# Performance work log

Measured on AMD Instinct MI355X. Metric: run time of the kernel, lower is better.

## Reference

```python
import jax, jax.numpy as jnp
import numpy as np

HID = 2560
NH, P, N, G, K = 80, 64, 128, 1, 4
INTER = NH * P            # 5120
CONV_DIM = INTER + 2 * G * N  # 5376
PROJ = INTER + CONV_DIM + NH  # 10576
EPS = 1e-5
DT_MIN, DT_MAX = 0.0, 100.0
BATCH = 64


def setup_inputs() -> dict:
    key = jax.random.key(0)
    ks = jax.random.split(key, 11)
    return {
        "input_states": jax.random.normal(ks[0], (BATCH, 1, HID), jnp.float32),
        "conv_state": 0.1 * jax.random.normal(ks[1], (BATCH, CONV_DIM, K), jnp.float32),
        "ssm_state": 0.1 * jax.random.normal(ks[2], (BATCH, NH, P, N), jnp.float32),
        "in_proj_w": jax.random.normal(ks[3], (PROJ, HID), jnp.float32) * (HID ** -0.5),
        "conv_w": jax.random.normal(ks[4], (CONV_DIM, K), jnp.float32) * 0.2,
        "conv_b": jax.random.normal(ks[5], (CONV_DIM,), jnp.float32) * 0.02,
        "dt_bias": jax.random.normal(ks[6], (NH,), jnp.float32) * 0.1,
        "A_log": jnp.log(jnp.arange(1, NH + 1, dtype=jnp.float32)),
        "D": jnp.ones((NH,), jnp.float32),
        "norm_w": jnp.ones((INTER,), jnp.float32),
        "out_proj_w": jax.random.normal(ks[7], (HID, INTER), jnp.float32) * (INTER ** -0.5),
    }


def reference(input_states, conv_state, ssm_state, in_proj_w, conv_w, conv_b,
              dt_bias, A_log, D, norm_w, out_proj_w):
    B = input_states.shape[0]
    # in_proj: (B,1,HID) @ (HID,PROJ) -> (B,1,PROJ); d_mlp == 0 with these dims
    proj = jnp.einsum("bsh,ph->bsp", input_states, in_proj_w)
    gate = proj[..., :INTER]                       # (B,1,INTER)
    hBC = proj[..., INTER:INTER + CONV_DIM]        # (B,1,CONV_DIM)
    dt = proj[..., INTER + CONV_DIM:]              # (B,1,NH)

    # conv cache update: roll left, append current token
    new_conv_state = jnp.concatenate(
        [conv_state[:, :, 1:], hBC[:, 0, :, None]], axis=-1)  # (B,CONV_DIM,K)
    x = jnp.sum(new_conv_state * conv_w[None], axis=-1) + conv_b  # (B,CONV_DIM)
    x = jax.nn.silu(x)

    hs = x[:, :INTER].reshape(B, NH, P)            # (B,NH,P)
    Bm = x[:, INTER:INTER + G * N].reshape(B, G, N)
    Cm = x[:, INTER + G * N:].reshape(B, G, N)
    Bm = jnp.repeat(Bm, NH // G, axis=1)           # (B,NH,N)
    Cm = jnp.repeat(Cm, NH // G, axis=1)           # (B,NH,N)

    # discretization (dt is per-head, broadcast over head_dim as in source)
    dt_sp = jnp.clip(jax.nn.softplus(dt[:, 0, :] + dt_bias), DT_MIN, DT_MAX)  # (B,NH)
    A = -jnp.exp(A_log)                            # (NH,)
    dA = jnp.exp(dt_sp * A)                        # (B,NH)

    dBx = dt_sp[:, :, None, None] * Bm[:, :, None, :] * hs[..., None]  # (B,NH,P,N)
    new_ssm = ssm_state * dA[:, :, None, None] + dBx                   # (B,NH,P,N)

    y = jnp.einsum("bhpn,bhn->bhp", new_ssm, Cm)   # (B,NH,P)
    y = y + hs * D[None, :, None]
    y = y.reshape(B, 1, INTER)

    # gated RMSNorm (fp32 internals)
    yf = y.astype(jnp.float32) * jax.nn.silu(gate.astype(jnp.float32))
    var = jnp.mean(yf * yf, axis=-1, keepdims=True)
    yn = norm_w * (yf * jax.lax.rsqrt(var + EPS)).astype(y.dtype)

    out = jnp.einsum("bsi,hi->bsh", yn, out_proj_w)  # (B,1,HID)
    return out
```

## Files before the change

### kernel.cpp

```cpp
#include <hip/hip_runtime.h>
#include <stdint.h>

#define HID 2560
#define NH 80
#define PDIM 64
#define NDIM 128
#define INTER 5120
#define CONV_DIM 5376
#define PROJ_DIM 10576
#define NBATCH 64
#define EPS_ 1e-5f

typedef short short8 __attribute__((ext_vector_type(8)));
typedef float f32x4 __attribute__((ext_vector_type(4)));

__device__ __forceinline__ unsigned short f2bf(float f){
  unsigned u = __builtin_bit_cast(unsigned, f);
  u += 0x7FFFu + ((u >> 16) & 1u);
  return (unsigned short)(u >> 16);
}
__device__ __forceinline__ float silu_(float x){ return x / (1.f + __expf(-x)); }

__global__ __launch_bounds__(256) void k_dt(const float* __restrict__ X,
                                            const float* __restrict__ W,
                                            float* __restrict__ dt_part,
                                            unsigned short* __restrict__ Xb){
  const int h = blockIdx.x, ks = blockIdx.y;
  const int tid = threadIdx.x, wid = tid >> 6, lane = tid & 63;
  const float* wr = W + (size_t)(INTER + CONV_DIM + h) * HID + ks * 320;
  float w[5];
  #pragma unroll
  for (int i = 0; i < 5; ++i) w[i] = wr[lane + i * 64];
  #pragma unroll
  for (int bi = 0; bi < 16; ++bi){
    const int b = wid * 16 + bi;
    const float* xr = X + (size_t)b * HID + ks * 320;
    float x[5];
    float acc = 0.f;
    #pragma unroll
    for (int i = 0; i < 5; ++i){ x[i] = xr[lane + i * 64]; acc += x[i] * w[i]; }
    if (h == 0){
      #pragma unroll
      for (int i = 0; i < 5; ++i)
        Xb[(size_t)b * HID + ks * 320 + lane + i * 64] = f2bf(x[i]);
    }
    #pragma unroll
    for (int m = 32; m; m >>= 1) acc += __shfl_xor(acc, m);
    if (lane == 0) dt_part[(ks * NBATCH + b) * NH + h] = acc;
  }
}

__global__ __launch_bounds__(64, 1) void k1_proj(const unsigned short* __restrict__ Xb,
                                                 const float* __restrict__ W,
                                                 float* __restrict__ pp){
  const int lane = threadIdx.x;
  const int lr = lane & 15, lg = lane >> 4;
  const int n0 = blockIdx.x * 16;
  const int ks = blockIdx.y;
  const int kb = ks * 640;
  const short* ap = (const short*)Xb + (size_t)lr * HID + kb + lg * 8;
  const float* bp = W + (size_t)(n0 + lr) * HID + kb + lg * 8;
  f32x4 acc0 = {0,0,0,0}, acc1 = {0,0,0,0}, acc2 = {0,0,0,0}, acc3 = {0,0,0,0};
  short8 A0[4], A1[4], A2[4], A3[4];
  float4 B0[4], B1[4];
  #pragma unroll
  for (int p = 0; p < 4; ++p){
    const int k = p * 32;
    A0[p] = *(const short8*)(ap + k);
    A1[p] = *(const short8*)(ap + 16 * HID + k);
    A2[p] = *(const short8*)(ap + 32 * HID + k);
    A3[p] = *(const short8*)(ap + 48 * HID + k);
    B0[p] = *(const float4*)(bp + k);
    B1[p] = *(const float4*)(bp + k + 4);
  }
  #pragma unroll 4
  for (int s = 0; s < 16; ++s){
    const int p = s & 3;
    short8 bb;
    bb[0]=(short)f2bf(B0[p].x); bb[1]=(short)f2bf(B0[p].y);
    bb[2]=(short)f2bf(B0[p].z); bb[3]=(short)f2bf(B0[p].w);
    bb[4]=(short)f2bf(B1[p].x); bb[5]=(short)f2bf(B1[p].y);
    bb[6]=(short)f2bf(B1[p].z); bb[7]=(short)f2bf(B1[p].w);
    acc0 = __builtin_amdgcn_mfma_f32_16x16x32_bf16(A0[p], bb, acc0, 0, 0, 0);
    acc1 = __builtin_amdgcn_mfma_f32_16x16x32_bf16(A1[p], bb, acc1, 0, 0, 0);
    acc2 = __builtin_amdgcn_mfma_f32_16x16x32_bf16(A2[p], bb, acc2, 0, 0, 0);
    acc3 = __builtin_amdgcn_mfma_f32_16x16x32_bf16(A3[p], bb, acc3, 0, 0, 0);
    const int k = (s + 4) * 32;
    A0[p] = *(const short8*)(ap + k);
    A1[p] = *(const short8*)(ap + 16 * HID + k);
    A2[p] = *(const short8*)(ap + 32 * HID + k);
    A3[p] = *(const short8*)(ap + 48 * HID + k);
    B0[p] = *(const float4*)(bp + k);
    B1[p] = *(const float4*)(bp + k + 4);
  }
  #pragma unroll
  for (int s = 16; s < 20; ++s){
    const int p = s & 3;
    short8 bb;
    bb[0]=(short)f2bf(B0[p].x); bb[1]=(short)f2bf(B0[p].y);
    bb[2]=(short)f2bf(B0[p].z); bb[3]=(short)f2bf(B0[p].w);
    bb[4]=(short)f2bf(B1[p].x); bb[5]=(short)f2bf(B1[p].y);
    bb[6]=(short)f2bf(B1[p].z); bb[7]=(short)f2bf(B1[p].w);
    acc0 = __builtin_amdgcn_mfma_f32_16x16x32_bf16(A0[p], bb, acc0, 0, 0, 0);
    acc1 = __builtin_amdgcn_mfma_f32_16x16x32_bf16(A1[p], bb, acc1, 0, 0, 0);
    acc2 = __builtin_amdgcn_mfma_f32_16x16x32_bf16(A2[p], bb, acc2, 0, 0, 0);
    acc3 = __builtin_amdgcn_mfma_f32_16x16x32_bf16(A3[p], bb, acc3, 0, 0, 0);
  }
  float* plane = pp + (size_t)ks * NBATCH * PROJ_DIM;
  #pragma unroll
  for (int r = 0; r < 4; ++r){
    const int m = lg * 4 + r;
    plane[(size_t)(m     ) * PROJ_DIM + n0 + lr] = acc0[r];
    plane[(size_t)(m + 16) * PROJ_DIM + n0 + lr] = acc1[r];
    plane[(size_t)(m + 32) * PROJ_DIM + n0 + lr] = acc2[r];
    plane[(size_t)(m + 48) * PROJ_DIM + n0 + lr] = acc3[r];
  }
}

__global__ __launch_bounds__(256) void k2a(const float* __restrict__ cs,
                                           const float* __restrict__ cw,
                                           const float* __restrict__ cb,
                                           const float* __restrict__ pp,
                                           const float* __restrict__ dt_part,
                                           const float* __restrict__ dt_bias,
                                           const float* __restrict__ A_log,
                                           float* __restrict__ hs_bc,
                                           float* __restrict__ dt_sp,
                                           float* __restrict__ dAv,
                                           float* __restrict__ s_bc){
  const int b = blockIdx.y;
  const int c0 = blockIdx.x * 384;
  const int tid = threadIdx.x;
  const size_t plane = (size_t)NBATCH * PROJ_DIM;
  __shared__ float bc[384];
  for (int i = tid; i < 384; i += 256){
    const int c = c0 + i;
    float4 s4 = *(const float4*)(cs + ((size_t)b * CONV_DIM + c) * 4);
    float4 w4 = *(const float4*)(cw + (size_t)c * 4);
    const size_t pidx = (size_t)b * PROJ_DIM + INTER + c;
    float hbc = pp[pidx] + pp[plane + pidx] + pp[2*plane + pidx] + pp[3*plane + pidx];
    float x = s4.y * w4.x + s4.z * w4.y + s4.w * w4.z + hbc * w4.w + cb[c];
    float v = silu_(x);
    hs_bc[(size_t)b * CONV_DIM + c] = v;
    if (blockIdx.x == 13) bc[i] = v;
  }
  if (blockIdx.x == 0 && tid < NH){
    float acc = dt_bias[tid];
    #pragma unroll
    for (int ks = 0; ks < 8; ++ks) acc += dt_part[(ks * NBATCH + b) * NH + tid];
    float sp = acc > 15.f ? acc : log1pf(__expf(acc));
    sp = fminf(fmaxf(sp, 0.f), 100.f);
    dt_sp[b * NH + tid] = sp;
    dAv[b * NH + tid] = __expf(-sp * __expf(A_log[tid]));
  }
  if (blockIdx.x == 13){
    __syncthreads();
    if (tid < 64){
      float p = bc[128 + tid] * bc[256 + tid] + bc[192 + tid] * bc[320 + tid];
      #pragma unroll
      for (int m = 32; m; m >>= 1) p += __shfl_xor(p, m);
      if (tid == 0) s_bc[b] = p;
    }
  }
}

__global__ __launch_bounds__(256) void k2b(const float* __restrict__ ssm,
                                           const float* __restrict__ hs_bc,
                                           const float* __restrict__ pp,
                                           const float* __restrict__ dt_sp,
                                           const float* __restrict__ dAv,
                                           const float* __restrict__ s_bc,
                                           const float* __restrict__ Dp,
                                           const float* __restrict__ norm_w,
                                           unsigned short* __restrict__ yfb,
                                           float* __restrict__ ssq_part){
  const int h = blockIdx.x, b = blockIdx.y;
  const int tid = threadIdx.x;
  const int wid = tid >> 6, lane = tid & 63;
  const int lr = lane & 15, lg = lane >> 4;
  const float dA_s = dAv[b * NH + h];
  const float coef = dt_sp[b * NH + h] * s_bc[b] + Dp[h];
  const size_t plane = (size_t)NBATCH * PROJ_DIM;
  const float* Cb = hs_bc + (size_t)b * CONV_DIM + INTER + NDIM;
  float4 c0 = *(const float4*)(Cb + lr * 8);
  float4 c1 = *(const float4*)(Cb + lr * 8 + 4);
  const float* srow = ssm + ((size_t)b * NH + h) * PDIM * NDIM;
  float ssq = 0.f;
  __shared__ float ssql[4];
  #pragma unroll
  for (int r = 0; r < 4; ++r){
    const int p = wid * 16 + r * 4 + lg;
    const float* sp_ = srow + (size_t)p * NDIM + lr * 8;
    float4 v0 = *(const float4*)(sp_);
    float4 v1 = *(const float4*)(sp_ + 4);
    float dot = v0.x*c0.x + v0.y*c0.y + v0.z*c0.z + v0.w*c0.w
              + v1.x*c1.x + v1.y*c1.y + v1.z*c1.z + v1.w*c1.w;
    dot += __shfl_xor(dot, 1); dot += __shfl_xor(dot, 2);
    dot += __shfl_xor(dot, 4); dot += __shfl_xor(dot, 8);
    if (lr == 0){
      const int hp = h * PDIM + p;
      float hs = hs_bc[(size_t)b * CONV_DIM + hp];
      float y = dA_s * dot + hs * coef;
      const size_t gi = (size_t)b * PROJ_DIM + hp;
      float g = pp[gi] + pp[plane + gi] + pp[2*plane + gi] + pp[3*plane + gi];
      float yf = y * silu_(g) * norm_w[hp];
      yfb[(size_t)b * INTER + hp] = f2bf(yf);
      ssq += yf * yf;
    }
  }
  #pragma unroll
  for (int m = 32; m; m >>= 1) ssq += __shfl_xor(ssq, m);
  if (lane == 0) ssql[wid] = ssq;
  __syncthreads();
  if (tid == 0) ssq_part[b * NH + h] = ssql[0] + ssql[1] + ssql[2] + ssql[3];
}

__global__ __launch_bounds__(64, 1) void k3_out(const unsigned short* __restrict__ Yb,
                                                const float* __restrict__ W,
                                                float* __restrict__ part){
  const int lane = threadIdx.x;
  const int lr = lane & 15, lg = lane >> 4;
  const int n0 = blockIdx.x * 16;
  const int ks = blockIdx.y;
  const int kb = ks * 1280;
  const short* ap = (const short*)Yb + (size_t)lr * INTER + kb + lg * 8;
  const float* bp = W + (size_t)(n0 + lr) * INTER + kb + lg * 8;
  f32x4 acc0 = {0,0,0,0}, acc1 = {0,0,0,0}, acc2 = {0,0,0,0}, acc3 = {0,0,0,0};
  short8 A0[4], A1[4], A2[4], A3[4];
  float4 B0[4], B1[4];
  #pragma unroll
  for (int p = 0; p < 4; ++p){
    const int k = p * 32;
    A0[p] = *(const short8*)(ap + k);
    A1[p] = *(const short8*)(ap + 16 * INTER + k);
    A2[p] = *(const short8*)(ap + 32 * INTER + k);
    A3[p] = *(const short8*)(ap + 48 * INTER + k);
    B0[p] = *(const float4*)(bp + k);
    B1[p] = *(const float4*)(bp + k + 4);
  }
  #pragma unroll 4
  for (int s = 0; s < 36; ++s){
    const int p = s & 3;
    short8 bb;
    bb[0]=(short)f2bf(B0[p].x); bb[1]=(short)f2bf(B0[p].y);
    bb[2]=(short)f2bf(B0[p].z); bb[3]=(short)f2bf(B0[p].w);
    bb[4]=(short)f2bf(B1[p].x); bb[5]=(short)f2bf(B1[p].y);
    bb[6]=(short)f2bf(B1[p].z); bb[7]=(short)f2bf(B1[p].w);
    acc0 = __builtin_amdgcn_mfma_f32_16x16x32_bf16(A0[p], bb, acc0, 0, 0, 0);
    acc1 = __builtin_amdgcn_mfma_f32_16x16x32_bf16(A1[p], bb, acc1, 0, 0, 0);
    acc2 = __builtin_amdgcn_mfma_f32_16x16x32_bf16(A2[p], bb, acc2, 0, 0, 0);
    acc3 = __builtin_amdgcn_mfma_f32_16x16x32_bf16(A3[p], bb, acc3, 0, 0, 0);
    const int k = (s + 4) * 32;
    A0[p] = *(const short8*)(ap + k);
    A1[p] = *(const short8*)(ap + 16 * INTER + k);
    A2[p] = *(const short8*)(ap + 32 * INTER + k);
    A3[p] = *(const short8*)(ap + 48 * INTER + k);
    B0[p] = *(const float4*)(bp + k);
    B1[p] = *(const float4*)(bp + k + 4);
  }
  #pragma unroll
  for (int s = 36; s < 40; ++s){
    const int p = s & 3;
    short8 bb;
    bb[0]=(short)f2bf(B0[p].x); bb[1]=(short)f2bf(B0[p].y);
    bb[2]=(short)f2bf(B0[p].z); bb[3]=(short)f2bf(B0[p].w);
    bb[4]=(short)f2bf(B1[p].x); bb[5]=(short)f2bf(B1[p].y);
    bb[6]=(short)f2bf(B1[p].z); bb[7]=(short)f2bf(B1[p].w);
    acc0 = __builtin_amdgcn_mfma_f32_16x16x32_bf16(A0[p], bb, acc0, 0, 0, 0);
    acc1 = __builtin_amdgcn_mfma_f32_16x16x32_bf16(A1[p], bb, acc1, 0, 0, 0);
    acc2 = __builtin_amdgcn_mfma_f32_16x16x32_bf16(A2[p], bb, acc2, 0, 0, 0);
    acc3 = __builtin_amdgcn_mfma_f32_16x16x32_bf16(A3[p], bb, acc3, 0, 0, 0);
  }
  float* pt = part + (size_t)ks * NBATCH * 2560;
  #pragma unroll
  for (int r = 0; r < 4; ++r){
    const int m = lg * 4 + r;
    pt[(size_t)(m     ) * 2560 + n0 + lr] = acc0[r];
    pt[(size_t)(m + 16) * 2560 + n0 + lr] = acc1[r];
    pt[(size_t)(m + 32) * 2560 + n0 + lr] = acc2[r];
    pt[(size_t)(m + 48) * 2560 + n0 + lr] = acc3[r];
  }
}

__global__ __launch_bounds__(256) void k4_norm(const float* __restrict__ part,
                                               const float* __restrict__ ssq_part,
                                               float* __restrict__ out){
  const int b = blockIdx.y;
  const int tid = threadIdx.x;
  __shared__ float w4[4];
  __shared__ float sc;
  float v = (tid < NH) ? ssq_part[b * NH + tid] : 0.f;
  #pragma unroll
  for (int m = 32; m; m >>= 1) v += __shfl_xor(v, m);
  const int wid = tid >> 6, lane = tid & 63;
  if (lane == 0) w4[wid] = v;
  __syncthreads();
  if (tid == 0){
    float total = w4[0] + w4[1] + w4[2] + w4[3];
    sc = rsqrtf(total / (float)INTER + EPS_);
  }
  __syncthreads();
  const int j = blockIdx.x * 256 + tid;
  const size_t idx = (size_t)b * 2560 + j;
  const size_t plane = (size_t)NBATCH * 2560;
  float s = part[idx] + part[plane + idx] + part[2*plane + idx] + part[3*plane + idx];
  out[idx] = sc * s;
}

extern "C" void kernel_launch(void* const* d_in, const int* in_sizes, int n_in,
                              void* d_out, int out_size, void* d_ws, size_t ws_size,
                              hipStream_t stream){
  const float* x_in       = (const float*)d_in[0];
  const float* conv_state = (const float*)d_in[1];
  const float* ssm_state  = (const float*)d_in[2];
  const float* in_proj_w  = (const float*)d_in[3];
  const float* conv_w     = (const float*)d_in[4];
  const float* conv_b     = (const float*)d_in[5];
  const float* dt_bias    = (const float*)d_in[6];
  const float* A_log      = (const float*)d_in[7];
  const float* Dp         = (const float*)d_in[8];
  const float* norm_w     = (const float*)d_in[9];
  const float* out_proj_w = (const float*)d_in[10];
  float* out = (float*)d_out;

  char* ws = (char*)d_ws;
  unsigned short* Xb   = (unsigned short*)(ws);
  float* dt_part       = (float*)(ws + 327680);
  float* pp            = (float*)(ws + 491520);
  float* hs_bc         = (float*)(ws + 11321344);
  float* dt_sp         = (float*)(ws + 12697600);
  float* dAv           = (float*)(ws + 12718080);
  float* s_bc          = (float*)(ws + 12738560);
  float* ssq           = (float*)(ws + 12738816);
  unsigned short* Yb   = (unsigned short*)(ws + 12759296);
  float* part          = (float*)(ws + 13414656);

  k_dt<<<dim3(NH, 8), dim3(256), 0, stream>>>(x_in, in_proj_w, dt_part, Xb);
  k1_proj<<<dim3(661, 4), dim3(64), 0, stream>>>(Xb, in_proj_w, pp);
  k2a<<<dim3(14, NBATCH), dim3(256), 0, stream>>>(conv_state, conv_w, conv_b, pp,
                                                  dt_part, dt_bias, A_log,
                                                  hs_bc, dt_sp, dAv, s_bc);
  k2b<<<dim3(NH, NBATCH), dim3(256), 0, stream>>>(ssm_state, hs_bc, pp, dt_sp, dAv,
                                                  s_bc, Dp, norm_w, Yb, ssq);
  k3_out<<<dim3(160, 4), dim3(64), 0, stream>>>(Yb, out_proj_w, part);
  k4_norm<<<dim3(10, NBATCH), dim3(256), 0, stream>>>(part, ssq, out);
}
```

Baseline: 134.6 us.

## Widen in_proj GEMM tiles to 64 columns and split K eight ways

Each in_proj wave now computes a 64x64 output tile (four N subtiles) instead of 64x16, so every A fragment load from Xb is reused across four weight subtiles. Split-K goes from 4 to 8 chunks of 320 to keep enough blocks (166x8), and the last tile clamps its weight rows and masks its stores. Consumers now sum eight partial planes, which doubles partial-sum traffic and workspace. Register pressure also rises with sixteen accumulators and double-buffered B loads.

```diff
diff --git a/kernel.cpp b/kernel.cpp
--- a/kernel.cpp
+++ b/kernel.cpp
@@ -55,65 +55,97 @@
                                                  float* __restrict__ pp){
   const int lane = threadIdx.x;
   const int lr = lane & 15, lg = lane >> 4;
-  const int n0 = blockIdx.x * 16;
+  const int n0 = blockIdx.x * 64;
   const int ks = blockIdx.y;
-  const int kb = ks * 640;
+  const int kb = ks * 320;
   const short* ap = (const short*)Xb + (size_t)lr * HID + kb + lg * 8;
-  const float* bp = W + (size_t)(n0 + lr) * HID + kb + lg * 8;
-  f32x4 acc0 = {0,0,0,0}, acc1 = {0,0,0,0}, acc2 = {0,0,0,0}, acc3 = {0,0,0,0};
-  short8 A0[4], A1[4], A2[4], A3[4];
-  float4 B0[4], B1[4];
-  #pragma unroll
-  for (int p = 0; p < 4; ++p){
-    const int k = p * 32;
-    A0[p] = *(const short8*)(ap + k);
-    A1[p] = *(const short8*)(ap + 16 * HID + k);
-    A2[p] = *(const short8*)(ap + 32 * HID + k);
-    A3[p] = *(const short8*)(ap + 48 * HID + k);
-    B0[p] = *(const float4*)(bp + k);
-    B1[p] = *(const float4*)(bp + k + 4);
-  }
-  #pragma unroll 4
-  for (int s = 0; s < 16; ++s){
-    const int p = s & 3;
-    short8 bb;
-    bb[0]=(short)f2bf(B0[p].x); bb[1]=(short)f2bf(B0[p].y);
-    bb[2]=(short)f2bf(B0[p].z); bb[3]=(short)f2bf(B0[p].w);
-    bb[4]=(short)f2bf(B1[p].x); bb[5]=(short)f2bf(B1[p].y);
-    bb[6]=(short)f2bf(B1[p].z); bb[7]=(short)f2bf(B1[p].w);
-    acc0 = __builtin_amdgcn_mfma_f32_16x16x32_bf16(A0[p], bb, acc0, 0, 0, 0);
-    acc1 = __builtin_amdgcn_mfma_f32_16x16x32_bf16(A1[p], bb, acc1, 0, 0, 0);
-    acc2 = __builtin_amdgcn_mfma_f32_16x16x32_bf16(A2[p], bb, acc2, 0, 0, 0);
-    acc3 = __builtin_amdgcn_mfma_f32_16x16x32_bf16(A3[p], bb, acc3, 0, 0, 0);
-    const int k = (s + 4) * 32;
-    A0[p] = *(const short8*)(ap + k);
-    A1[p] = *(const short8*)(ap + 16 * HID + k);
-    A2[p] = *(const short8*)(ap + 32 * HID + k);
-    A3[p] = *(const short8*)(ap + 48 * HID + k);
-    B0[p] = *(const float4*)(bp + k);
-    B1[p] = *(const float4*)(bp + k + 4);
-  }
-  #pragma unroll
-  for (int s = 16; s < 20; ++s){
-    const int p = s & 3;
-    short8 bb;
-    bb[0]=(short)f2bf(B0[p].x); bb[1]=(short)f2bf(B0[p].y);
-    bb[2]=(short)f2bf(B0[p].z); bb[3]=(short)f2bf(B0[p].w);
-    bb[4]=(short)f2bf(B1[p].x); bb[5]=(short)f2bf(B1[p].y);
-    bb[6]=(short)f2bf(B1[p].z); bb[7]=(short)f2bf(B1[p].w);
-    acc0 = __builtin_amdgcn_mfma_f32_16x16x32_bf16(A0[p], bb, acc0, 0, 0, 0);
-    acc1 = __builtin_amdgcn_mfma_f32_16x16x32_bf16(A1[p], bb, acc1, 0, 0, 0);
-    acc2 = __builtin_amdgcn_mfma_f32_16x16x32_bf16(A2[p], bb, acc2, 0, 0, 0);
-    acc3 = __builtin_amdgcn_mfma_f32_16x16x32_bf16(A3[p], bb, acc3, 0, 0, 0);
+  const float* bp0; const float* bp1; const float* bp2; const float* bp3;
+  {
+    int r0 = n0;          if (r0 > PROJ_DIM - 16) r0 = PROJ_DIM - 16;
+    int r1 = n0 + 16;     if (r1 > PROJ_DIM - 16) r1 = PROJ_DIM - 16;
+    int r2 = n0 + 32;     if (r2 > PROJ_DIM - 16) r2 = PROJ_DIM - 16;
+    int r3 = n0 + 48;     if (r3 > PROJ_DIM - 16) r3 = PROJ_DIM - 16;
+    bp0 = W + (size_t)(r0 + lr) * HID + kb + lg * 8;
+    bp1 = W + (size_t)(r1 + lr) * HID + kb + lg * 8;
+    bp2 = W + (size_t)(r2 + lr) * HID + kb + lg * 8;
+    bp3 = W + (size_t)(r3 + lr) * HID + kb + lg * 8;
+  }
+  f32x4 acc0[4], acc1[4], acc2[4], acc3[4];
+  #pragma unroll
+  for (int mt = 0; mt < 4; ++mt){
+    acc0[mt] = (f32x4){0,0,0,0}; acc1[mt] = (f32x4){0,0,0,0};
+    acc2[mt] = (f32x4){0,0,0,0}; acc3[mt] = (f32x4){0,0,0,0};
+  }
+  short8 A0[2], A1[2], A2[2], A3[2];
+  float4 Bv0[2][2], Bv1[2][2], Bv2[2][2], Bv3[2][2];
+  A0[0] = *(const short8*)(ap);
+  A1[0] = *(const short8*)(ap + 16 * HID);
+  A2[0] = *(const short8*)(ap + 32 * HID);
+  A3[0] = *(const short8*)(ap + 48 * HID);
+  Bv0[0][0] = *(const float4*)(bp0); Bv0[0][1] = *(const float4*)(bp0 + 4);
+  Bv1[0][0] = *(const float4*)(bp1); Bv1[0][1] = *(const float4*)(bp1 + 4);
+  Bv2[0][0] = *(const float4*)(bp2); Bv2[0][1] = *(const float4*)(bp2 + 4);
+  Bv3[0][0] = *(const float4*)(bp3); Bv3[0][1] = *(const float4*)(bp3 + 4);
+  #pragma unroll
+  for (int s = 0; s < 10; ++s){
+    const int p = s & 1;
+    if (s + 1 < 10){
+      const int k = (s + 1) * 32, q = p ^ 1;
+      A0[q] = *(const short8*)(ap + k);
+      A1[q] = *(const short8*)(ap + 16 * HID + k);
+      A2[q] = *(const short8*)(ap + 32 * HID + k);
+      A3[q] = *(const short8*)(ap + 48 * HID + k);
+      Bv0[q][0] = *(const float4*)(bp0 + k); Bv0[q][1] = *(const float4*)(bp0 + k + 4);
+      Bv1[q][0] = *(const float4*)(bp1 + k); Bv1[q][1] = *(const float4*)(bp1 + k + 4);
+      Bv2[q][0] = *(const float4*)(bp2 + k); Bv2[q][1] = *(const float4*)(bp2 + k + 4);
+      Bv3[q][0] = *(const float4*)(bp3 + k); Bv3[q][1] = *(const float4*)(bp3 + k + 4);
+    }
+    short8 bb0, bb1, bb2, bb3;
+    bb0[0]=(short)f2bf(Bv0[p][0].x); bb0[1]=(short)f2bf(Bv0[p][0].y);
+    bb0[2]=(short)f2bf(Bv0[p][0].z); bb0[3]=(short)f2bf(Bv0[p][0].w);
+    bb0[4]=(short)f2bf(Bv0[p][1].x); bb0[5]=(short)f2bf(Bv0[p][1].y);
+    bb0[6]=(short)f2bf(Bv0[p][1].z); bb0[7]=(short)f2bf(Bv0[p][1].w);
+    bb1[0]=(short)f2bf(Bv1[p][0].x); bb1[1]=(short)f2bf(Bv1[p][0].y);
+    bb1[2]=(short)f2bf(Bv1[p][0].z); bb1[3]=(short)f2bf(Bv1[p][0].w);
+    bb1[4]=(short)f2bf(Bv1[p][1].x); bb1[5]=(short)f2bf(Bv1[p][1].y);
+    bb1[6]=(short)f2bf(Bv1[p][1].z); bb1[7]=(short)f2bf(Bv1[p][1].w);
+    bb2[0]=(short)f2bf(Bv2[p][0].x); bb2[1]=(short)f2bf(Bv2[p][0].y);
+    bb2[2]=(short)f2bf(Bv2[p][0].z); bb2[3]=(short)f2bf(Bv2[p][0].w);
+    bb2[4]=(short)f2bf(Bv2[p][1].x); bb2[5]=(short)f2bf(Bv2[p][1].y);
+    bb2[6]=(short)f2bf(Bv2[p][1].z); bb2[7]=(short)f2bf(Bv2[p][1].w);
+    bb3[0]=(short)f2bf(Bv3[p][0].x); bb3[1]=(short)f2bf(Bv3[p][0].y);
+    bb3[2]=(short)f2bf(Bv3[p][0].z); bb3[3]=(short)f2bf(Bv3[p][0].w);
+    bb3[4]=(short)f2bf(Bv3[p][1].x); bb3[5]=(short)f2bf(Bv3[p][1].y);
+    bb3[6]=(short)f2bf(Bv3[p][1].z); bb3[7]=(short)f2bf(Bv3[p][1].w);
+    acc0[0] = __builtin_amdgcn_mfma_f32_16x16x32_bf16(A0[p], bb0, acc0[0], 0, 0, 0);
+    acc0[1] = __builtin_amdgcn_mfma_f32_16x16x32_bf16(A1[p], bb0, acc0[1], 0, 0, 0);
+    acc0[2] = __builtin_amdgcn_mfma_f32_16x16x32_bf16(A2[p], bb0, acc0[2], 0, 0, 0);
+    acc0[3] = __builtin_amdgcn_mfma_f32_16x16x32_bf16(A3[p], bb0, acc0[3], 0, 0, 0);
+    acc1[0] = __builtin_amdgcn_mfma_f32_16x16x32_bf16(A0[p], bb1, acc1[0], 0, 0, 0);
+    acc1[1] = __builtin_amdgcn_mfma_f32_16x16x32_bf16(A1[p], bb1, acc1[1], 0, 0, 0);
+    acc1[2] = __builtin_amdgcn_mfma_f32_16x16x32_bf16(A2[p], bb1, acc1[2], 0, 0, 0);
+    acc1[3] = __builtin_amdgcn_mfma_f32_16x16x32_bf16(A3[p], bb1, acc1[3], 0, 0, 0);
+    acc2[0] = __builtin_amdgcn_mfma_f32_16x16x32_bf16(A0[p], bb2, acc2[0], 0, 0, 0);
+    acc2[1] = __builtin_amdgcn_mfma_f32_16x16x32_bf16(A1[p], bb2, acc2[1], 0, 0, 0);
+    acc2[2] = __builtin_amdgcn_mfma_f32_16x16x32_bf16(A2[p], bb2, acc2[2], 0, 0, 0);
+    acc2[3] = __builtin_amdgcn_mfma_f32_16x16x32_bf16(A3[p], bb2, acc2[3], 0, 0, 0);
+    acc3[0] = __builtin_amdgcn_mfma_f32_16x16x32_bf16(A0[p], bb3, acc3[0], 0, 0, 0);
+    acc3[1] = __builtin_amdgcn_mfma_f32_16x16x32_bf16(A1[p], bb3, acc3[1], 0, 0, 0);
+    acc3[2] = __builtin_amdgcn_mfma_f32_16x16x32_bf16(A2[p], bb3, acc3[2], 0, 0, 0);
+    acc3[3] = __builtin_amdgcn_mfma_f32_16x16x32_bf16(A3[p], bb3, acc3[3], 0, 0, 0);
   }
   float* plane = pp + (size_t)ks * NBATCH * PROJ_DIM;
   #pragma unroll
-  for (int r = 0; r < 4; ++r){
-    const int m = lg * 4 + r;
-    plane[(size_t)(m     ) * PROJ_DIM + n0 + lr] = acc0[r];
-    plane[(size_t)(m + 16) * PROJ_DIM + n0 + lr] = acc1[r];
-    plane[(size_t)(m + 32) * PROJ_DIM + n0 + lr] = acc2[r];
-    plane[(size_t)(m + 48) * PROJ_DIM + n0 + lr] = acc3[r];
+  for (int mt = 0; mt < 4; ++mt){
+    #pragma unroll
+    for (int r = 0; r < 4; ++r){
+      const int m = mt * 16 + lg * 4 + r;
+      float* pm = plane + (size_t)m * PROJ_DIM;
+      if (n0      < PROJ_DIM) pm[n0      + lr] = acc0[mt][r];
+      if (n0 + 16 < PROJ_DIM) pm[n0 + 16 + lr] = acc1[mt][r];
+      if (n0 + 32 < PROJ_DIM) pm[n0 + 32 + lr] = acc2[mt][r];
+      if (n0 + 48 < PROJ_DIM) pm[n0 + 48 + lr] = acc3[mt][r];
+    }
   }
 }
 
@@ -138,7 +170,9 @@
     float4 s4 = *(const float4*)(cs + ((size_t)b * CONV_DIM + c) * 4);
     float4 w4 = *(const float4*)(cw + (size_t)c * 4);
     const size_t pidx = (size_t)b * PROJ_DIM + INTER + c;
-    float hbc = pp[pidx] + pp[plane + pidx] + pp[2*plane + pidx] + pp[3*plane + pidx];
+    float hbc = 0.f;
+    #pragma unroll
+    for (int ks = 0; ks < 8; ++ks) hbc += pp[(size_t)ks * plane + pidx];
     float x = s4.y * w4.x + s4.z * w4.y + s4.w * w4.z + hbc * w4.w + cb[c];
     float v = silu_(x);
     hs_bc[(size_t)b * CONV_DIM + c] = v;
@@ -202,7 +236,9 @@
       float hs = hs_bc[(size_t)b * CONV_DIM + hp];
       float y = dA_s * dot + hs * coef;
       const size_t gi = (size_t)b * PROJ_DIM + hp;
-      float g = pp[gi] + pp[plane + gi] + pp[2*plane + gi] + pp[3*plane + gi];
+      float g = 0.f;
+      #pragma unroll
+      for (int ks = 0; ks < 8; ++ks) g += pp[(size_t)ks * plane + gi];
       float yf = y * silu_(g) * norm_w[hp];
       yfb[(size_t)b * INTER + hp] = f2bf(yf);
       ssq += yf * yf;
@@ -327,16 +363,16 @@
   unsigned short* Xb   = (unsigned short*)(ws);
   float* dt_part       = (float*)(ws + 327680);
   float* pp            = (float*)(ws + 491520);
-  float* hs_bc         = (float*)(ws + 11321344);
-  float* dt_sp         = (float*)(ws + 12697600);
-  float* dAv           = (float*)(ws + 12718080);
-  float* s_bc          = (float*)(ws + 12738560);
-  float* ssq           = (float*)(ws + 12738816);
-  unsigned short* Yb   = (unsigned short*)(ws + 12759296);
-  float* part          = (float*)(ws + 13414656);
+  float* hs_bc         = (float*)(ws + 22151168);
+  float* dt_sp         = (float*)(ws + 23527424);
+  float* dAv           = (float*)(ws + 23547904);
+  float* s_bc          = (float*)(ws + 23568384);
+  float* ssq           = (float*)(ws + 23568640);
+  unsigned short* Yb   = (unsigned short*)(ws + 23589120);
+  float* part          = (float*)(ws + 24244480);
 
   k_dt<<<dim3(NH, 8), dim3(256), 0, stream>>>(x_in, in_proj_w, dt_part, Xb);
-  k1_proj<<<dim3(661, 4), dim3(64), 0, stream>>>(Xb, in_proj_w, pp);
+  k1_proj<<<dim3(166, 8), dim3(64), 0, stream>>>(Xb, in_proj_w, pp);
   k2a<<<dim3(14, NBATCH), dim3(256), 0, stream>>>(conv_state, conv_w, conv_b, pp,
                                                   dt_part, dt_bias, A_log,
                                                   hs_bc, dt_sp, dAv, s_bc);
```

Result: faster. 127.5 us (-5.3%).
